# Performance work log

Measured on AMD Instinct MI355X. Metric: run time of the kernel, lower is better.

The kernel has to match this reference:

```python
import jax, jax.numpy as jnp
import numpy as np

N_LAYERS = 4
D_MODEL = 64        # 8*8 hardcoded in source
D_STATE = 128
D_CONV = 4
EXPAND = 2
HEADDIM = 64        # Mamba2Simple default
D_INNER = EXPAND * D_MODEL            # 128
NHEADS = D_INNER // HEADDIM           # 2
NGROUPS = 1
D_IN_PROJ = 2 * D_INNER + 2 * NGROUPS * D_STATE + NHEADS   # 514
CONV_DIM = D_INNER + 2 * NGROUPS * D_STATE                 # 384
EPS = 1e-5
B_SZ, SEQ = 8, 4096


def setup_inputs() -> dict:
    key = jax.random.key(0)
    ks = jax.random.split(key, 8)
    s = 0.02
    x = jax.random.normal(ks[0], (B_SZ, SEQ, D_MODEL), jnp.float32)
    in_proj_w = jax.random.normal(ks[1], (N_LAYERS, D_IN_PROJ, D_MODEL), jnp.float32) * s
    conv_w = jax.random.normal(ks[2], (N_LAYERS, CONV_DIM, 1, D_CONV), jnp.float32) * 0.2
    conv_b = jnp.zeros((N_LAYERS, CONV_DIM), jnp.float32)
    # dt_bias ~ inverse-softplus of small dt values
    dt_bias = jax.random.uniform(ks[3], (N_LAYERS, NHEADS), jnp.float32, -4.0, 0.0)
    A_log = jnp.log(jax.random.uniform(ks[4], (N_LAYERS, NHEADS), jnp.float32, 1.0, 16.0))
    D = jnp.ones((N_LAYERS, NHEADS), jnp.float32)
    norm_w = jnp.ones((N_LAYERS, D_INNER), jnp.float32)
    out_proj_w = jax.random.normal(ks[5], (N_LAYERS, D_MODEL, D_INNER), jnp.float32) * s
    return {"x": x, "in_proj_w": in_proj_w, "conv_w": conv_w, "conv_b": conv_b,
            "dt_bias": dt_bias, "A_log": A_log, "D": D, "norm_w": norm_w,
            "out_proj_w": out_proj_w}


def _ssm(xh, dt, A, Bm, Cm):
    """Selective-scan SSM. xh:(B,L,H,P) dt:(B,L,H) A:(H,) Bm,Cm:(B,L,S) -> (B,L,H,P)"""
    dA = jnp.exp(dt * A)  # (B,L,H)

    def step(h, inp):
        dA_t, dt_t, x_t, B_t, C_t = inp
        # h: (B,H,P,S)
        h = h * dA_t[:, :, None, None] + (dt_t[:, :, None] * x_t)[..., None] * B_t[:, None, None, :]
        y = jnp.einsum('bhps,bs->bhp', h, C_t)
        return h, y

    b = xh.shape[0]
    h0 = jnp.zeros((b, NHEADS, HEADDIM, D_STATE), xh.dtype)
    xs = (jnp.moveaxis(dA, 1, 0), jnp.moveaxis(dt, 1, 0), jnp.moveaxis(xh, 1, 0),
          jnp.moveaxis(Bm, 1, 0), jnp.moveaxis(Cm, 1, 0))
    _, ys = jax.lax.scan(step, h0, xs)
    return jnp.moveaxis(ys, 0, 1)


def _layer(x, p):
    in_w, cw, cb, dtb, Alog, Dp, nw, ow = p
    zxbcdt = x @ in_w.T                                   # (B,L,514)
    z = zxbcdt[..., :D_INNER]
    xBC = zxbcdt[..., D_INNER:D_INNER + CONV_DIM]
    dt = jax.nn.softplus(zxbcdt[..., -NHEADS:] + dtb)     # (B,L,H)
    # causal depthwise conv over sequence
    xc = jnp.moveaxis(xBC, -1, 1)                         # (B,C,L)
    xc = jax.lax.conv_general_dilated(xc, cw, (1,), [(D_CONV - 1, 0)],
                                      dimension_numbers=('NCH', 'OIH', 'NCH'),
                                      feature_group_count=CONV_DIM)
    xBC = jax.nn.silu(jnp.moveaxis(xc + cb[None, :, None], 1, -1))
    xs = xBC[..., :D_INNER]
    Bm = xBC[..., D_INNER:D_INNER + D_STATE]
    Cm = xBC[..., D_INNER + D_STATE:]
    xh = xs.reshape(xs.shape[0], xs.shape[1], NHEADS, HEADDIM)
    A = -jnp.exp(Alog)                                    # (H,)
    y = _ssm(xh, dt, A, Bm, Cm) + Dp[None, None, :, None] * xh
    y = y.reshape(y.shape[0], y.shape[1], D_INNER)
    # gated RMSNorm (norm_before_gate=False): rmsnorm(y * silu(z)) * w
    y = y * jax.nn.silu(z)
    y = y * jax.lax.rsqrt(jnp.mean(y * y, axis=-1, keepdims=True) + EPS) * nw
    return y @ ow.T


def reference(x, in_proj_w, conv_w, conv_b, dt_bias, A_log, D, norm_w, out_proj_w):
    def body(xc, p):
        return _layer(xc, p) + xc, None
    out, _ = jax.lax.scan(body, x, (in_proj_w, conv_w, conv_b, dt_bias, A_log, D, norm_w, out_proj_w))
    return out
```

## Files before the change

### kernel.cpp

```cpp
#include <hip/hip_runtime.h>
#include <math.h>

#define B_SZ 8
#define SEQ  4096
#define DM   64
#define DI   128
#define NH   2
#define HD   64
#define DS   128
#define DIP  514
#define ZW   512
#define CD   384
#define QC   64
#define NC   64
#define NR   (B_SZ*SEQ)
#define WPAD 576

typedef __attribute__((ext_vector_type(8))) short bf16x8;
typedef __attribute__((ext_vector_type(4))) float f32x4;

__device__ __forceinline__ unsigned short f2bf(float f) {
    union { float f; unsigned int u; } x; x.f = f;
    unsigned int r = x.u + 0x7fffu + ((x.u >> 16) & 1u);
    return (unsigned short)(r >> 16);
}
__device__ __forceinline__ float bf2f(unsigned short h) {
    union { unsigned int u; float f; } x; x.u = ((unsigned int)h) << 16;
    return x.f;
}
__device__ __forceinline__ bf16x8 fragld(const unsigned short* base, int r0, int k0, int ld) {
    int l = threadIdx.x & 63;
    return *(const bf16x8*)(base + (size_t)(r0 + (l & 15)) * ld + k0 + (l >> 4) * 8);
}

__global__ __launch_bounds__(256) void k_wcvt(const float* __restrict__ in_w,
                                              const float* __restrict__ out_w,
                                              unsigned short* __restrict__ Wb,
                                              unsigned short* __restrict__ OWb) {
    int idx = blockIdx.x * 256 + threadIdx.x;
    if (idx < 4 * WPAD * 64) {
        int l = idx / (WPAD * 64), r = idx % (WPAD * 64);
        int n = r >> 6, k = r & 63;
        float v = (n < DIP) ? in_w[(size_t)l * DIP * 64 + (size_t)n * 64 + k] : 0.f;
        Wb[idx] = f2bf(v);
    }
    if (idx < 4 * 64 * 128) OWb[idx] = f2bf(out_w[idx]);
}

__global__ __launch_bounds__(256) void k_xcvt(const float* __restrict__ X,
                                              unsigned short* __restrict__ Xb) {
    int idx = (blockIdx.x * 256 + threadIdx.x) * 4;
    float4 v = *(const float4*)(X + idx);
    uint2 p;
    p.x = f2bf(v.x) | ((unsigned int)f2bf(v.y) << 16);
    p.y = f2bf(v.z) | ((unsigned int)f2bf(v.w) << 16);
    *(uint2*)(Xb + idx) = p;
}

__global__ __launch_bounds__(256) void k_inproj(const unsigned short* __restrict__ Xb,
                                                const unsigned short* __restrict__ Wb,
                                                unsigned short* __restrict__ ZXb,
                                                float* __restrict__ DT) {
    int m0 = blockIdx.x * 256;
    int n0 = blockIdx.y * 64;
    int tid = threadIdx.x;
    int wid = tid >> 6, lane = tid & 63;
    int q4 = lane >> 4, c16 = lane & 15;
    int mb = m0 + wid * 64;
    bf16x8 af[4][2];
#pragma unroll
    for (int mt = 0; mt < 4; mt++)
#pragma unroll
        for (int ks = 0; ks < 2; ks++)
            af[mt][ks] = *(const bf16x8*)(Xb + (size_t)(mb + mt * 16 + c16) * 64 + ks * 32 + q4 * 8);
    if (n0 < 512) {
#pragma unroll
        for (int nt = 0; nt < 4; nt++) {
            bf16x8 bf[2];
#pragma unroll
            for (int ks = 0; ks < 2; ks++)
                bf[ks] = *(const bf16x8*)(Wb + (size_t)(n0 + nt * 16 + c16) * 64 + ks * 32 + q4 * 8);
#pragma unroll
            for (int mt = 0; mt < 4; mt++) {
                f32x4 acc = {0.f, 0.f, 0.f, 0.f};
                acc = __builtin_amdgcn_mfma_f32_16x16x32_bf16(af[mt][0], bf[0], acc, 0, 0, 0);
                acc = __builtin_amdgcn_mfma_f32_16x16x32_bf16(af[mt][1], bf[1], acc, 0, 0, 0);
#pragma unroll
                for (int rr = 0; rr < 4; rr++) {
                    float v = acc[rr];
                    float vn = __shfl_xor(v, 1);
                    if (!(lane & 1)) {
                        unsigned int pk = f2bf(v) | ((unsigned int)f2bf(vn) << 16);
                        *(unsigned int*)(ZXb + (size_t)(mb + mt * 16 + q4 * 4 + rr) * ZW + n0 + nt * 16 + c16) = pk;
                    }
                }
            }
        }
    } else {
        bf16x8 bf[2];
#pragma unroll
        for (int ks = 0; ks < 2; ks++)
            bf[ks] = *(const bf16x8*)(Wb + (size_t)(512 + c16) * 64 + ks * 32 + q4 * 8);
#pragma unroll
        for (int mt = 0; mt < 4; mt++) {
            f32x4 acc = {0.f, 0.f, 0.f, 0.f};
            acc = __builtin_amdgcn_mfma_f32_16x16x32_bf16(af[mt][0], bf[0], acc, 0, 0, 0);
            acc = __builtin_amdgcn_mfma_f32_16x16x32_bf16(af[mt][1], bf[1], acc, 0, 0, 0);
            if (c16 < 2)
#pragma unroll
                for (int rr = 0; rr < 4; rr++)
                    DT[(size_t)(mb + mt * 16 + q4 * 4 + rr) * 2 + c16] = acc[rr];
        }
    }
}

__global__ __launch_bounds__(512, 4) void k_chunk1(
        const unsigned short* __restrict__ ZXb, const float* __restrict__ DT,
        const float* __restrict__ CW, const float* __restrict__ CB,
        const float* __restrict__ dtb, const float* __restrict__ Alog,
        const float* __restrict__ Dv,
        unsigned short* __restrict__ SL, unsigned short* __restrict__ ECB,
        float* __restrict__ TB, unsigned short* __restrict__ YBb) {
    __shared__ unsigned short sBt[128][72];
    __shared__ unsigned short sXt[128][72];
    __shared__ unsigned short uBC[2][64][136];
    __shared__ float s_cum[2][64], s_dt[2][64], s_w[2][64], s_e[2][64];
    unsigned short (*sM)[64][72] = (unsigned short (*)[64][72])&uBC[0][0][0];

    int c = blockIdx.x, b = blockIdx.y;
    size_t rbase = (size_t)b * SEQ + c * QC;
    int tid = threadIdx.x;
    int wid = tid >> 6, lane = tid & 63;

    if (wid < 2) {
        int h = wid, j = lane;
        float raw = DT[(rbase + j) * 2 + h] + dtb[h];
        float dt = (raw > 20.f) ? raw : log1pf(__expf(raw));
        float A = -__expf(Alog[h]);
        float x = dt * A;
        for (int off = 1; off < 64; off <<= 1) {
            float o = __shfl_up(x, off);
            if (lane >= off) x += o;
        }
        float T = __shfl(x, 63);
        s_dt[h][j] = dt;
        s_cum[h][j] = x;
        s_w[h][j] = __expf(T - x) * dt;
        s_e[h][j] = __expf(x);
        if (j == 0) TB[(b * 2 + h) * NC + c] = __expf(T);
    }
    __syncthreads();

    size_t ecbase = ((size_t)(b * NC + c)) * 2 * 8192;
    for (int e = tid; e < 64 * 96; e += 512) {
        int j = e / 96;
        int q = e - j * 96;
        int cc = q * 4;
        int l = c * QC + j;
        const unsigned short* zp = ZXb + (rbase + j) * ZW + 128 + cc;
        uint2 a0 = *(const uint2*)zp;
        uint2 a1 = make_uint2(0, 0), a2 = make_uint2(0, 0), a3 = make_uint2(0, 0);
        if (l >= 1) a1 = *(const uint2*)(zp - ZW);
        if (l >= 2) a2 = *(const uint2*)(zp - 2 * ZW);
        if (l >= 3) a3 = *(const uint2*)(zp - 3 * ZW);
        float v[4];
#pragma unroll
        for (int u = 0; u < 4; u++) {
            unsigned int w0 = (u < 2) ? a0.x : a0.y;
            unsigned int w1 = (u < 2) ? a1.x : a1.y;
            unsigned int w2 = (u < 2) ? a2.x : a2.y;
            unsigned int w3 = (u < 2) ? a3.x : a3.y;
            int sh = (u & 1) * 16;
            float r0 = bf2f((unsigned short)(w0 >> sh));
            float r1 = bf2f((unsigned short)(w1 >> sh));
            float r2 = bf2f((unsigned short)(w2 >> sh));
            float r3 = bf2f((unsigned short)(w3 >> sh));
            float4 wv = *(const float4*)(CW + (cc + u) * 4);
            float t = CB[cc + u] + wv.w * r0 + wv.z * r1 + wv.y * r2 + wv.x * r3;
            v[u] = t / (1.f + __expf(-t));
        }
        if (cc < 128) {
#pragma unroll
            for (int u = 0; u < 4; u++) sXt[cc + u][j] = f2bf(v[u]);
        } else if (cc < 256) {
            int s = cc - 128;
            unsigned int p0 = f2bf(v[0]) | ((unsigned int)f2bf(v[1]) << 16);
            unsigned int p1 = f2bf(v[2]) | ((unsigned int)f2bf(v[3]) << 16);
            *(uint2*)&uBC[0][j][s] = make_uint2(p0, p1);
#pragma unroll
            for (int u = 0; u < 4; u++) sBt[s + u][j] = f2bf(v[u]);
        } else {
            int s = cc - 256;
            unsigned int p0 = f2bf(v[0]) | ((unsigned int)f2bf(v[1]) << 16);
            unsigned int p1 = f2bf(v[2]) | ((unsigned int)f2bf(v[3]) << 16);
            *(uint2*)&uBC[1][j][s] = make_uint2(p0, p1);
            float e0 = s_e[0][j], e1 = s_e[1][j];
            unsigned int q0 = f2bf(v[0] * e0) | ((unsigned int)f2bf(v[1] * e0) << 16);
            unsigned int q1 = f2bf(v[2] * e0) | ((unsigned int)f2bf(v[3] * e0) << 16);
            *(uint2*)(ECB + ecbase + (size_t)j * 128 + s) = make_uint2(q0, q1);
            q0 = f2bf(v[0] * e1) | ((unsigned int)f2bf(v[1] * e1) << 16);
            q1 = f2bf(v[2] * e1) | ((unsigned int)f2bf(v[3] * e1) << 16);
            *(uint2*)(ECB + ecbase + 8192 + (size_t)j * 128 + s) = make_uint2(q0, q1);
        }
    }
    __syncthreads();

    int q4 = lane >> 4, c16 = lane & 15;
    f32x4 gacc[2];
#pragma unroll
    for (int u = 0; u < 2; u++) {
        int t = wid * 2 + u;
        int it = t >> 2, jt = t & 3;
        f32x4 acc = {0.f, 0.f, 0.f, 0.f};
        for (int ks = 0; ks < 4; ks++) {
            bf16x8 a = fragld(&uBC[1][0][0], it * 16, ks * 32, 136);
            bf16x8 bb = fragld(&uBC[0][0][0], jt * 16, ks * 32, 136);
            acc = __builtin_amdgcn_mfma_f32_16x16x32_bf16(a, bb, acc, 0, 0, 0);
        }
        gacc[u] = acc;
    }
    __syncthreads();
#pragma unroll
    for (int u = 0; u < 2; u++) {
        int t = wid * 2 + u;
        int it = t >> 2, jt = t & 3;
        int j = jt * 16 + c16;
        for (int rr = 0; rr < 4; rr++) {
            int i = it * 16 + q4 * 4 + rr;
            float gv = gacc[u][rr];
            for (int h = 0; h < 2; h++) {
                float m = 0.f;
                if (j <= i) m = gv * __expf(s_cum[h][i] - s_cum[h][j]) * s_dt[h][j];
                sM[h][i][j] = f2bf(m);
            }
        }
    }
    __syncthreads();

#pragma unroll
    for (int u = 0; u < 4; u++) {
        int idx = wid * 4 + u;
        int h = idx >> 4, tt = idx & 15;
        int it = tt >> 2, pt = tt & 3;
        float dco = Dv[h];
        int pg = h * 64 + pt * 16 + c16;
        f32x4 acc;
        for (int rr = 0; rr < 4; rr++) {
            int i = it * 16 + q4 * 4 + rr;
            acc[rr] = dco * bf2f(sXt[pg][i]);
        }
        for (int ks = 0; ks < 2; ks++) {
            bf16x8 a = fragld(&sM[h][0][0], it * 16, ks * 32, 72);
            bf16x8 bb = fragld(&sXt[0][0], h * 64 + pt * 16, ks * 32, 72);
            acc = __builtin_amdgcn_mfma_f32_16x16x32_bf16(a, bb, acc, 0, 0, 0);
        }
        for (int rr = 0; rr < 4; rr++) {
            int i = it * 16 + q4 * 4 + rr;
            float v = acc[rr];
            float vn = __shfl_xor(v, 1);
            if (!(lane & 1)) {
                unsigned int pk = f2bf(v) | ((unsigned int)f2bf(vn) << 16);
                *(unsigned int*)(YBb + (rbase + i) * DI + pg) = pk;
            }
        }
    }
    size_t slbase = ((size_t)(b * NC + c)) * 16384;
#pragma unroll
    for (int u = 0; u < 8; u++) {
        int idx = wid * 8 + u;
        int ptl = idx >> 3, st = idx & 7;
        int h = ptl >> 2;
        f32x4 acc = {0.f, 0.f, 0.f, 0.f};
        for (int ks = 0; ks < 2; ks++) {
            int jb = ks * 32 + (lane >> 4) * 8;
            bf16x8 a = fragld(&sXt[0][0], ptl * 16, ks * 32, 72);
            bf16x8 aw;
#pragma unroll
            for (int t = 0; t < 8; t++) aw[t] = (short)f2bf(bf2f((unsigned short)a[t]) * s_w[h][jb + t]);
            bf16x8 bb = fragld(&sBt[0][0], st * 16, ks * 32, 72);
            acc = __builtin_amdgcn_mfma_f32_16x16x32_bf16(aw, bb, acc, 0, 0, 0);
        }
        int s = st * 16 + c16;
        for (int rr = 0; rr < 4; rr++) {
            int p = ptl * 16 + q4 * 4 + rr;
            float vv = acc[rr];
            float vn = __shfl_xor(vv, 1);
            if (!(lane & 1)) {
                unsigned int pk = f2bf(vv) | ((unsigned int)f2bf(vn) << 16);
                *(unsigned int*)(SL + slbase + (size_t)p * 128 + s) = pk;
            }
        }
    }
}

__global__ __launch_bounds__(256) void k_scan(unsigned short* __restrict__ SL,
                                              const float* __restrict__ TB) {
    int bid = blockIdx.x;
    int b = bid >> 6;
    int ps = (bid & 63) * 256 + threadIdx.x;
    int h = ps >> 13;
    const float* dAp = TB + (b * 2 + h) * NC;
    size_t base = (size_t)(b * NC) * 16384 + ps;
    float hacc = 0.f;
#pragma unroll 8
    for (int cc = 0; cc < NC; cc++) {
        size_t idx = base + (size_t)cc * 16384;
        float slv = bf2f(SL[idx]);
        SL[idx] = f2bf(hacc);
        hacc = hacc * dAp[cc] + slv;
    }
}

__global__ __launch_bounds__(512, 2) void k_fused(
        const unsigned short* __restrict__ SL, const unsigned short* __restrict__ ECB,
        const unsigned short* __restrict__ YBb, const unsigned short* __restrict__ ZXb,
        const float* __restrict__ NW, const unsigned short* __restrict__ OWb,
        float* __restrict__ XR, unsigned short* __restrict__ Xbn) {
    __shared__ __attribute__((aligned(16))) unsigned short sH[128][136];
    __shared__ __attribute__((aligned(16))) unsigned short sE[128][136];
    float* sGf = (float*)&sH[0][0];
    unsigned short (*sG)[136] = (unsigned short (*)[136])&sE[0][0];

    int c = blockIdx.x, b = blockIdx.y;
    size_t rbase = (size_t)b * SEQ + c * QC;
    int tid = threadIdx.x;
    int wid = tid >> 6, lane = tid & 63;
    size_t base = ((size_t)(b * NC + c)) * 16384;
    for (int u = 0; u < 4; u++) {
        int e = u * 512 + tid;
        int row = e >> 4, cb8 = (e & 15) * 8;
        *(uint4*)&sH[row][cb8] = *(const uint4*)(SL + base + (size_t)row * 128 + cb8);
        *(uint4*)&sE[row][cb8] = *(const uint4*)(ECB + base + (size_t)row * 128 + cb8);
    }
    __syncthreads();
    int q4 = lane >> 4, c16 = lane & 15;

    float yv[4][4];
    int tit[4], tpg[4];
#pragma unroll
    for (int u = 0; u < 4; u++) {
        int idx = wid * 4 + u;
        int h = idx >> 4, tt = idx & 15;
        int it = tt >> 2, pt = tt & 3;
        f32x4 acc = {0.f, 0.f, 0.f, 0.f};
        for (int ks = 0; ks < 4; ks++) {
            bf16x8 a = fragld(&sE[0][0], h * 64 + it * 16, ks * 32, 136);
            bf16x8 bb = fragld(&sH[0][0], h * 64 + pt * 16, ks * 32, 136);
            acc = __builtin_amdgcn_mfma_f32_16x16x32_bf16(a, bb, acc, 0, 0, 0);
        }
        int pg = h * 64 + pt * 16 + c16;
        tit[u] = it; tpg[u] = pg;
        for (int rr = 0; rr < 4; rr++) {
            int i = it * 16 + q4 * 4 + rr;
            float y = acc[rr] + bf2f(YBb[(rbase + i) * DI + pg]);
            float z = bf2f(ZXb[(rbase + i) * ZW + pg]);
            yv[u][rr] = y * (z / (1.f + __expf(-z)));
        }
    }
    __syncthreads();
#pragma unroll
    for (int u = 0; u < 4; u++)
        for (int rr = 0; rr < 4; rr++) {
            int i = tit[u] * 16 + q4 * 4 + rr;
            sGf[i * 132 + tpg[u]] = yv[u][rr];
        }
    __syncthreads();
    {
        int row = tid >> 3, p0 = (tid & 7) * 16;
        float g[16];
        float ss = 0.f;
        for (int t2 = 0; t2 < 16; t2++) { g[t2] = sGf[row * 132 + p0 + t2]; ss += g[t2] * g[t2]; }
        ss += __shfl_xor(ss, 1);
        ss += __shfl_xor(ss, 2);
        ss += __shfl_xor(ss, 4);
        float rms = rsqrtf(ss * (1.f / 128.f) + 1e-5f);
        for (int t2 = 0; t2 < 16; t2 += 2) {
            unsigned int pk = f2bf(g[t2] * rms * NW[p0 + t2]) |
                              ((unsigned int)f2bf(g[t2 + 1] * rms * NW[p0 + t2 + 1]) << 16);
            *(unsigned int*)&sG[row][p0 + t2] = pk;
        }
    }
    __syncthreads();
#pragma unroll
    for (int u = 0; u < 2; u++) {
        int t = wid * 2 + u;
        int mt = t >> 2, nt = t & 3;
        f32x4 acc = {0.f, 0.f, 0.f, 0.f};
        for (int ks = 0; ks < 4; ks++) {
            bf16x8 a = fragld(&sG[0][0], mt * 16, ks * 32, 136);
            bf16x8 bb = *(const bf16x8*)(OWb + (size_t)(nt * 16 + c16) * 128 + ks * 32 + q4 * 8);
            acc = __builtin_amdgcn_mfma_f32_16x16x32_bf16(a, bb, acc, 0, 0, 0);
        }
        for (int rr = 0; rr < 4; rr++) {
            int m = mt * 16 + q4 * 4 + rr;
            int n = nt * 16 + c16;
            size_t o = (rbase + m) * DM + n;
            float v = XR[o] + acc[rr];
            XR[o] = v;
            float vn = __shfl_xor(v, 1);
            if (!(lane & 1)) {
                unsigned int pk = f2bf(v) | ((unsigned int)f2bf(vn) << 16);
                *(unsigned int*)(Xbn + o) = pk;
            }
        }
    }
}

extern "C" void kernel_launch(void* const* d_in, const int* in_sizes, int n_in,
                              void* d_out, int out_size, void* d_ws, size_t ws_size,
                              hipStream_t stream) {
    const float* x       = (const float*)d_in[0];
    const float* in_w    = (const float*)d_in[1];
    const float* conv_w  = (const float*)d_in[2];
    const float* conv_b  = (const float*)d_in[3];
    const float* dt_bias = (const float*)d_in[4];
    const float* A_log   = (const float*)d_in[5];
    const float* Dp      = (const float*)d_in[6];
    const float* norm_w  = (const float*)d_in[7];
    const float* out_w   = (const float*)d_in[8];
    float* out = (float*)d_out;
    float* ws  = (float*)d_ws;

    float* dt = ws;
    float* tb = dt + (size_t)NR * 2;
    unsigned short* zxb = (unsigned short*)(tb + 1024);
    unsigned short* ybb = zxb + (size_t)NR * ZW;
    unsigned short* sl  = ybb + (size_t)NR * DI;
    unsigned short* ecb = sl + (size_t)B_SZ * NC * 16384;
    unsigned short* xb  = ecb + (size_t)B_SZ * NC * 16384;
    unsigned short* wb  = xb + (size_t)NR * DM;
    unsigned short* owb = wb + (size_t)4 * WPAD * 64;

    k_wcvt<<<(4 * WPAD * 64 + 255) / 256, 256, 0, stream>>>(in_w, out_w, wb, owb);
    k_xcvt<<<NR * DM / 1024, 256, 0, stream>>>(x, xb);
    hipMemcpyAsync(out, x, (size_t)NR * DM * sizeof(float), hipMemcpyDeviceToDevice, stream);

    for (int layer = 0; layer < 4; layer++) {
        k_inproj<<<dim3(NR / 256, 9), 256, 0, stream>>>(xb, wb + (size_t)layer * WPAD * 64, zxb, dt);
        k_chunk1<<<dim3(NC, B_SZ), 512, 0, stream>>>(zxb, dt,
                conv_w + (size_t)layer * CD * 4, conv_b + (size_t)layer * CD,
                dt_bias + layer * NH, A_log + layer * NH, Dp + layer * NH,
                sl, ecb, tb, ybb);
        k_scan<<<512, 256, 0, stream>>>(sl, tb);
        k_fused<<<dim3(NC, B_SZ), 512, 0, stream>>>(sl, ecb, ybb, zxb,
                norm_w + layer * DI, owb + (size_t)layer * 64 * 128, out, xb);
    }
}
```

Baseline: 384.8 us.

## Store raw C plus per-row decay instead of pre-scaled EC; keep residual in bf16

Result: faster. 370.3 us (-3.8%).

```diff
diff --git a/kernel.cpp b/kernel.cpp
--- a/kernel.cpp
+++ b/kernel.cpp
@@ -119,12 +119,13 @@
         const float* __restrict__ CW, const float* __restrict__ CB,
         const float* __restrict__ dtb, const float* __restrict__ Alog,
         const float* __restrict__ Dv,
-        unsigned short* __restrict__ SL, unsigned short* __restrict__ ECB,
+        unsigned short* __restrict__ SL, unsigned short* __restrict__ CBuf,
+        float* __restrict__ EB,
         float* __restrict__ TB, unsigned short* __restrict__ YBb) {
     __shared__ unsigned short sBt[128][72];
     __shared__ unsigned short sXt[128][72];
     __shared__ unsigned short uBC[2][64][136];
-    __shared__ float s_cum[2][64], s_dt[2][64], s_w[2][64], s_e[2][64];
+    __shared__ float s_cum[2][64], s_dt[2][64], s_w[2][64];
     unsigned short (*sM)[64][72] = (unsigned short (*)[64][72])&uBC[0][0][0];
 
     int c = blockIdx.x, b = blockIdx.y;
@@ -146,12 +147,12 @@
         s_dt[h][j] = dt;
         s_cum[h][j] = x;
         s_w[h][j] = __expf(T - x) * dt;
-        s_e[h][j] = __expf(x);
+        EB[((size_t)(b * NC + c)) * 128 + h * 64 + j] = __expf(x);
         if (j == 0) TB[(b * 2 + h) * NC + c] = __expf(T);
     }
     __syncthreads();
 
-    size_t ecbase = ((size_t)(b * NC + c)) * 2 * 8192;
+    size_t cbbase = ((size_t)(b * NC + c)) * 8192;
     for (int e = tid; e < 64 * 96; e += 512) {
         int j = e / 96;
         int q = e - j * 96;
@@ -194,13 +195,7 @@
             unsigned int p0 = f2bf(v[0]) | ((unsigned int)f2bf(v[1]) << 16);
             unsigned int p1 = f2bf(v[2]) | ((unsigned int)f2bf(v[3]) << 16);
             *(uint2*)&uBC[1][j][s] = make_uint2(p0, p1);
-            float e0 = s_e[0][j], e1 = s_e[1][j];
-            unsigned int q0 = f2bf(v[0] * e0) | ((unsigned int)f2bf(v[1] * e0) << 16);
-            unsigned int q1 = f2bf(v[2] * e0) | ((unsigned int)f2bf(v[3] * e0) << 16);
-            *(uint2*)(ECB + ecbase + (size_t)j * 128 + s) = make_uint2(q0, q1);
-            q0 = f2bf(v[0] * e1) | ((unsigned int)f2bf(v[1] * e1) << 16);
-            q1 = f2bf(v[2] * e1) | ((unsigned int)f2bf(v[3] * e1) << 16);
-            *(uint2*)(ECB + ecbase + 8192 + (size_t)j * 128 + s) = make_uint2(q0, q1);
+            *(uint2*)(CBuf + cbbase + (size_t)j * 128 + s) = make_uint2(p0, p1);
         }
     }
     __syncthreads();
@@ -312,10 +307,11 @@
 }
 
 __global__ __launch_bounds__(512, 2) void k_fused(
-        const unsigned short* __restrict__ SL, const unsigned short* __restrict__ ECB,
+        const unsigned short* __restrict__ SL, const unsigned short* __restrict__ CBuf,
+        const float* __restrict__ EB,
         const unsigned short* __restrict__ YBb, const unsigned short* __restrict__ ZXb,
         const float* __restrict__ NW, const unsigned short* __restrict__ OWb,
-        float* __restrict__ XR, unsigned short* __restrict__ Xbn) {
+        unsigned short* __restrict__ Xb, float* __restrict__ OutF, int last) {
     __shared__ __attribute__((aligned(16))) unsigned short sH[128][136];
     __shared__ __attribute__((aligned(16))) unsigned short sE[128][136];
     float* sGf = (float*)&sH[0][0];
@@ -330,7 +326,27 @@
         int e = u * 512 + tid;
         int row = e >> 4, cb8 = (e & 15) * 8;
         *(uint4*)&sH[row][cb8] = *(const uint4*)(SL + base + (size_t)row * 128 + cb8);
-        *(uint4*)&sE[row][cb8] = *(const uint4*)(ECB + base + (size_t)row * 128 + cb8);
+    }
+    size_t cbbase = ((size_t)(b * NC + c)) * 8192;
+    size_t ebase  = ((size_t)(b * NC + c)) * 128;
+    for (int u = 0; u < 2; u++) {
+        int idx8 = u * 512 + tid;
+        int i = idx8 >> 4, sc = (idx8 & 15) * 8;
+        uint4 cv = *(const uint4*)(CBuf + cbbase + (size_t)i * 128 + sc);
+        float e0 = EB[ebase + i], e1 = EB[ebase + 64 + i];
+        unsigned int w[4] = {cv.x, cv.y, cv.z, cv.w};
+        uint4 o0, o1;
+        unsigned int* po0 = &o0.x;
+        unsigned int* po1 = &o1.x;
+#pragma unroll
+        for (int t = 0; t < 4; t++) {
+            float lo = bf2f((unsigned short)(w[t] & 0xffff));
+            float hi = bf2f((unsigned short)(w[t] >> 16));
+            po0[t] = f2bf(lo * e0) | ((unsigned int)f2bf(hi * e0) << 16);
+            po1[t] = f2bf(lo * e1) | ((unsigned int)f2bf(hi * e1) << 16);
+        }
+        *(uint4*)&sE[i][sc] = o0;
+        *(uint4*)&sE[64 + i][sc] = o1;
     }
     __syncthreads();
     int q4 = lane >> 4, c16 = lane & 15;
@@ -395,12 +411,15 @@
             int m = mt * 16 + q4 * 4 + rr;
             int n = nt * 16 + c16;
             size_t o = (rbase + m) * DM + n;
-            float v = XR[o] + acc[rr];
-            XR[o] = v;
-            float vn = __shfl_xor(v, 1);
-            if (!(lane & 1)) {
-                unsigned int pk = f2bf(v) | ((unsigned int)f2bf(vn) << 16);
-                *(unsigned int*)(Xbn + o) = pk;
+            float v = bf2f(Xb[o]) + acc[rr];
+            if (last) {
+                OutF[o] = v;
+            } else {
+                float vn = __shfl_xor(v, 1);
+                if (!(lane & 1)) {
+                    unsigned int pk = f2bf(v) | ((unsigned int)f2bf(vn) << 16);
+                    *(unsigned int*)(Xb + o) = pk;
+                }
             }
         }
     }
@@ -423,26 +442,27 @@
 
     float* dt = ws;
     float* tb = dt + (size_t)NR * 2;
-    unsigned short* zxb = (unsigned short*)(tb + 1024);
-    unsigned short* ybb = zxb + (size_t)NR * ZW;
-    unsigned short* sl  = ybb + (size_t)NR * DI;
-    unsigned short* ecb = sl + (size_t)B_SZ * NC * 16384;
-    unsigned short* xb  = ecb + (size_t)B_SZ * NC * 16384;
-    unsigned short* wb  = xb + (size_t)NR * DM;
-    unsigned short* owb = wb + (size_t)4 * WPAD * 64;
+    float* eb = tb + 1024;
+    unsigned short* zxb  = (unsigned short*)(eb + (size_t)B_SZ * NC * 128);
+    unsigned short* ybb  = zxb + (size_t)NR * ZW;
+    unsigned short* sl   = ybb + (size_t)NR * DI;
+    unsigned short* cbuf = sl + (size_t)B_SZ * NC * 16384;
+    unsigned short* xb   = cbuf + (size_t)B_SZ * NC * 8192;
+    unsigned short* wb   = xb + (size_t)NR * DM;
+    unsigned short* owb  = wb + (size_t)4 * WPAD * 64;
 
     k_wcvt<<<(4 * WPAD * 64 + 255) / 256, 256, 0, stream>>>(in_w, out_w, wb, owb);
     k_xcvt<<<NR * DM / 1024, 256, 0, stream>>>(x, xb);
-    hipMemcpyAsync(out, x, (size_t)NR * DM * sizeof(float), hipMemcpyDeviceToDevice, stream);
 
     for (int layer = 0; layer < 4; layer++) {
         k_inproj<<<dim3(NR / 256, 9), 256, 0, stream>>>(xb, wb + (size_t)layer * WPAD * 64, zxb, dt);
         k_chunk1<<<dim3(NC, B_SZ), 512, 0, stream>>>(zxb, dt,
                 conv_w + (size_t)layer * CD * 4, conv_b + (size_t)layer * CD,
                 dt_bias + layer * NH, A_log + layer * NH, Dp + layer * NH,
-                sl, ecb, tb, ybb);
+                sl, cbuf, eb, tb, ybb);
         k_scan<<<512, 256, 0, stream>>>(sl, tb);
-        k_fused<<<dim3(NC, B_SZ), 512, 0, stream>>>(sl, ecb, ybb, zxb,
-                norm_w + layer * DI, owb + (size_t)layer * 64 * 128, out, xb);
-    }
-}
+        k_fused<<<dim3(NC, B_SZ), 512, 0, stream>>>(sl, cbuf, eb, ybb, zxb,
+                norm_w + layer * DI, owb + (size_t)layer * 64 * 128, xb, out,
+                (layer == 3) ? 1 : 0);
+    }
+}
```
